# Performance work log

Hardware: AMD Instinct MI355X
Metric: run time of the kernel (lower is better)

## Reference

```python
import jax, jax.numpy as jnp
import numpy as np

GAMMA = 2.0  # focal loss focusing parameter
N, C = 1048576, 80


def setup_inputs() -> dict:
    key = jax.random.key(0)
    k1, k2 = jax.random.split(key)
    inp = jax.random.normal(k1, (N, C), dtype=jnp.float32)
    target = jax.random.randint(k2, (N,), 0, C, dtype=jnp.int64)
    return {"input": inp, "target": target}


def reference(input, target):
    n, c = input.shape
    # sign mask: +1 at the target class, -1 elsewhere (replaces the Python loop)
    tgt_onehot = jax.nn.one_hot(target, c, dtype=input.dtype)  # [N, C]
    sign = 2.0 * tgt_onehot - 1.0
    x = input * sign
    logpt = jax.nn.log_sigmoid(x)                              # [N, C]
    # pt is detached in the original (Variable(logpt.data.exp()))
    pt = jax.lax.stop_gradient(jnp.exp(logpt))
    loss = -((1.0 - pt) ** GAMMA) * logpt                      # [N, C]
    loss = loss.sum(axis=1)                                    # [N]
    return loss.mean()  # reduction='mean'
```

## Files before the change

kernel.cpp:

```cpp
#include <hip/hip_runtime.h>


#define FL_N 1048576
#define FL_C 80
#define FL_VEC_PER_ROW (FL_C / 4)

__global__ __launch_bounds__(256) void focal_loss_kernel(
    const float* __restrict__ inp,
    const int* __restrict__ tgt,
    float* __restrict__ out,
    int nvec)
{
    const float inv_n = 1.0f / (float)FL_N;
    float acc = 0.0f;

    int stride = gridDim.x * blockDim.x;
    for (int f = blockIdx.x * blockDim.x + threadIdx.x; f < nvec; f += stride) {
        float4 v = reinterpret_cast<const float4*>(inp)[f];
        int r = f / FL_VEC_PER_ROW;
        int cbase = (f - r * FL_VEC_PER_ROW) * 4;
        int t = tgt[r];

        float vals[4] = {v.x, v.y, v.z, v.w};
        #pragma unroll
        for (int k = 0; k < 4; ++k) {
            float xv = vals[k];
            float x = ((cbase + k) == t) ? xv : -xv;
            float ax    = fabsf(x);
            float e     = __expf(-ax);
            float denom = 1.0f + e;
            float logpt = fminf(x, 0.0f) - __logf(denom);
            float pt    = ((x >= 0.0f) ? 1.0f : e) / denom;
            float omp   = 1.0f - pt;
            acc += omp * omp * (-logpt);
        }
    }

    #pragma unroll
    for (int off = 32; off > 0; off >>= 1)
        acc += __shfl_down(acc, off, 64);

    __shared__ float ws[4];
    int lane = threadIdx.x & 63;
    int wid  = threadIdx.x >> 6;
    if (lane == 0) ws[wid] = acc;
    __syncthreads();
    if (threadIdx.x == 0) {
        float s = ws[0] + ws[1] + ws[2] + ws[3];
        atomicAdd(out, s * inv_n);
    }
}

extern "C" void kernel_launch(void* const* d_in, const int* in_sizes, int n_in,
                              void* d_out, int out_size, void* d_ws, size_t ws_size,
                              hipStream_t stream) {
    const float* inp = (const float*)d_in[0];
    const int*   tgt = (const int*)d_in[1];
    float*       out = (float*)d_out;

    int nvec = (FL_N * FL_C) / 4;

    hipMemsetAsync(out, 0, sizeof(float), stream);

    dim3 grid(2048), block(256);
    focal_loss_kernel<<<grid, block, 0, stream>>>(inp, tgt, out, nvec);
}
```

Measured before the change: 449.0 us.

## Simplify focal loss math and unroll fixed-count loop with nontemporal loads

Rewrites the per-element focal loss as sigmoid(-x)^2 * log(1+exp(-x)), using one exp, one hardware reciprocal and one log instead of abs, select and division. The grid-stride loop becomes a compile-time trip count unrolled by four, with nontemporal vector loads and two accumulators. The aim is to cut ALU and latency costs in a streaming reduction. The unguarded exp can overflow for large-magnitude inputs, which changes numerical robustness.

```diff
diff --git a/kernel.cpp b/kernel.cpp
--- a/kernel.cpp
+++ b/kernel.cpp
@@ -1,53 +1,58 @@
 #include <hip/hip_runtime.h>
 
 
-#define FL_N 1048576
-#define FL_C 80
-#define FL_VEC_PER_ROW (FL_C / 4)
+#define FL_N      1048576
+#define FL_C      80
+#define FL_NVEC   (FL_N * FL_C / 4)
+#define FL_BLOCKS 2048
+#define FL_TPB    256
+#define FL_STRIDE (FL_BLOCKS * FL_TPB)
+#define FL_ITERS  (FL_NVEC / FL_STRIDE)
 
-__global__ __launch_bounds__(256) void focal_loss_kernel(
+typedef float floatx4 __attribute__((ext_vector_type(4)));
+
+__global__ __launch_bounds__(FL_TPB) void focal_loss_kernel(
     const float* __restrict__ inp,
     const int* __restrict__ tgt,
-    float* __restrict__ out,
-    int nvec)
+    float* __restrict__ out)
 {
-    const float inv_n = 1.0f / (float)FL_N;
-    float acc = 0.0f;
+    const floatx4* inp4 = reinterpret_cast<const floatx4*>(inp);
+    const int f0 = blockIdx.x * FL_TPB + threadIdx.x;
 
-    int stride = gridDim.x * blockDim.x;
-    for (int f = blockIdx.x * blockDim.x + threadIdx.x; f < nvec; f += stride) {
-        float4 v = reinterpret_cast<const float4*>(inp)[f];
-        int r = f / FL_VEC_PER_ROW;
-        int cbase = (f - r * FL_VEC_PER_ROW) * 4;
-        int t = tgt[r];
+    float acc0 = 0.0f, acc1 = 0.0f;
 
-        float vals[4] = {v.x, v.y, v.z, v.w};
+    #pragma unroll 4
+    for (int i = 0; i < FL_ITERS; ++i) {
+        int f = f0 + i * FL_STRIDE;
+        floatx4 v = __builtin_nontemporal_load(&inp4[f]);
+        int r  = f / 20;
+        int dt = tgt[r] - (f - r * 20) * 4;
+
         #pragma unroll
         for (int k = 0; k < 4; ++k) {
-            float xv = vals[k];
-            float x = ((cbase + k) == t) ? xv : -xv;
-            float ax    = fabsf(x);
-            float e     = __expf(-ax);
-            float denom = 1.0f + e;
-            float logpt = fminf(x, 0.0f) - __logf(denom);
-            float pt    = ((x >= 0.0f) ? 1.0f : e) / denom;
-            float omp   = 1.0f - pt;
-            acc += omp * omp * (-logpt);
+            float nx = (k == dt) ? -v[k] : v[k];
+            float u  = __expf(nx);
+            float d  = 1.0f + u;
+            float rc = __builtin_amdgcn_rcpf(d);
+            float lg = __logf(d);
+            float w  = u * rc;
+            if (k & 1) acc1 = fmaf(w * w, lg, acc1);
+            else       acc0 = fmaf(w * w, lg, acc0);
         }
     }
+
+    float acc = acc0 + acc1;
 
     #pragma unroll
     for (int off = 32; off > 0; off >>= 1)
         acc += __shfl_down(acc, off, 64);
 
     __shared__ float ws[4];
-    int lane = threadIdx.x & 63;
-    int wid  = threadIdx.x >> 6;
-    if (lane == 0) ws[wid] = acc;
+    if ((threadIdx.x & 63) == 0) ws[threadIdx.x >> 6] = acc;
     __syncthreads();
     if (threadIdx.x == 0) {
         float s = ws[0] + ws[1] + ws[2] + ws[3];
-        atomicAdd(out, s * inv_n);
+        atomicAdd(out, s * (1.0f / (float)FL_N));
     }
 }
 
@@ -58,10 +63,7 @@
     const int*   tgt = (const int*)d_in[1];
     float*       out = (float*)d_out;
 
-    int nvec = (FL_N * FL_C) / 4;
+    (void)hipMemsetAsync(out, 0, sizeof(float), stream);
 
-    hipMemsetAsync(out, 0, sizeof(float), stream);
-
-    dim3 grid(2048), block(256);
-    focal_loss_kernel<<<grid, block, 0, stream>>>(inp, tgt, out, nvec);
+    focal_loss_kernel<<<dim3(FL_BLOCKS), dim3(FL_TPB), 0, stream>>>(inp, tgt, out);
 }
```

After: 426.1 us. -5.1%, faster.
